# Optimization experiments

Hardware: AMD Instinct MI355X
Metric: run time of the kernel (lower is better)

The kernel has to match this reference:

```python
import jax, jax.numpy as jnp
import numpy as np

D_MODEL = 2048
D_FF = 8192
N_LOCAL = 8192


def _ffn(x, W1, b1, W2, b2):
    # ExpertFFN: Linear -> GELU(exact, torch default) -> Linear
    h = jax.nn.gelu(x @ W1 + b1, approximate=False)
    return h @ W2 + b2


def setup_inputs() -> dict:
    key = jax.random.key(0)
    ks = jax.random.split(key, 12)
    s1 = 1.0 / np.sqrt(D_MODEL)
    s2 = 1.0 / np.sqrt(D_FF)
    inp = {
        "x_local": jax.random.normal(ks[0], (N_LOCAL, D_MODEL), jnp.float32),
        "top2_exp_id": jax.random.randint(ks[1], (N_LOCAL, 2), 0, 2),
        "top2_weight": jax.random.uniform(ks[2], (N_LOCAL, 2), jnp.float32),
        # expert 0 params
        "W1_0": jax.random.uniform(ks[3], (D_MODEL, D_FF), jnp.float32, -s1, s1),
        "b1_0": jax.random.uniform(ks[4], (D_FF,), jnp.float32, -s1, s1),
        "W2_0": jax.random.uniform(ks[5], (D_FF, D_MODEL), jnp.float32, -s2, s2),
        "b2_0": jax.random.uniform(ks[6], (D_MODEL,), jnp.float32, -s2, s2),
        # expert 1 params
        "W1_1": jax.random.uniform(ks[7], (D_MODEL, D_FF), jnp.float32, -s1, s1),
        "b1_1": jax.random.uniform(ks[8], (D_FF,), jnp.float32, -s1, s1),
        "W2_1": jax.random.uniform(ks[9], (D_FF, D_MODEL), jnp.float32, -s2, s2),
        "b2_1": jax.random.uniform(ks[10], (D_MODEL,), jnp.float32, -s2, s2),
    }
    return inp


def reference(x_local, top2_exp_id, top2_weight,
              W1_0, b1_0, W2_0, b2_0, W1_1, b1_1, W2_1, b2_1):
    # Single-rank semantics of MoETop2TwoExpertsPerRank (world_size=1):
    # every token is dispatched to its two chosen local experts (ids in {0,1})
    # and results are combined weighted by the gate weights.
    y0 = _ffn(x_local, W1_0, b1_0, W2_0, b2_0)  # (N, d_model)
    y1 = _ffn(x_local, W1_1, b1_1, W2_1, b2_1)  # (N, d_model)
    # local expert id = global_eid % 2 (EPR=2); select per (token, slot)
    sel = (top2_exp_id % 2)[..., None].astype(x_local.dtype)  # (N, 2, 1)
    ys = jnp.stack([y0, y1], axis=1)  # not needed; use where instead
    per_slot = (1.0 - sel) * y0[:, None, :] + sel * y1[:, None, :]  # (N,2,d)
    y_out = jnp.sum(top2_weight[..., None] * per_slot, axis=1)
    return y_out
```

## Files before the change

kernel.cpp:

```cpp
#include <hip/hip_runtime.h>
#include <hip/hip_bf16.h>
#include <stdint.h>

#define DM 2048
#define DF 8192
#define NT 8192

typedef unsigned short u16;
typedef __attribute__((ext_vector_type(8))) __bf16 bf16x8;
typedef __attribute__((ext_vector_type(4))) float f32x4;

typedef __attribute__((address_space(1))) uint8_t ga_u8_t;
typedef __attribute__((address_space(3))) uint8_t lds_u8_t;

__device__ __forceinline__ void async_cp16(const void* g, void* l) {
  __builtin_amdgcn_global_load_lds((ga_u8_t*)g, (lds_u8_t*)l, 16, 0, 0);
}

__device__ __forceinline__ u16 f2b(float f) {
  unsigned int u = __builtin_bit_cast(unsigned int, f);
  u = (u + 0x7fffu + ((u >> 16) & 1u)) >> 16;
  return (u16)u;
}
__device__ __forceinline__ float gelu_f(float x) {
  return 0.5f * x * (1.0f + erff(x * 0.70710678118654752f));
}

__global__ void prep_wtok(const int* __restrict__ eid, const float* __restrict__ w,
                          float2* __restrict__ wtok, int n) {
  int i = blockIdx.x * blockDim.x + threadIdx.x;
  if (i >= n) return;
  float a = 0.f, b = 0.f;
  int e0 = eid[2 * i] & 1, e1 = eid[2 * i + 1] & 1;
  float w0 = w[2 * i], w1 = w[2 * i + 1];
  if (e0) b += w0; else a += w0;
  if (e1) b += w1; else a += w1;
  wtok[i] = make_float2(a, b);
}

__global__ void conv_f32_bf16(const float* __restrict__ in, u16* __restrict__ out,
                              int n4) {
  int i = blockIdx.x * blockDim.x + threadIdx.x;
  if (i >= n4) return;
  float4 v = reinterpret_cast<const float4*>(in)[i];
  ushort4 o;
  o.x = f2b(v.x); o.y = f2b(v.y); o.z = f2b(v.z); o.w = f2b(v.w);
  reinterpret_cast<ushort4*>(out)[i] = o;
}

__global__ void transpose_conv(const float* __restrict__ in, u16* __restrict__ out,
                               int R, int Cc) {
  __shared__ float tile[32][33];
  int tx = threadIdx.x & 31, ty = threadIdx.x >> 5;
  int r0 = blockIdx.y * 32, c0 = blockIdx.x * 32;
#pragma unroll
  for (int i = 0; i < 32; i += 8)
    tile[ty + i][tx] = in[(size_t)(r0 + ty + i) * Cc + c0 + tx];
  __syncthreads();
#pragma unroll
  for (int i = 0; i < 32; i += 8)
    out[(size_t)(c0 + ty + i) * R + r0 + tx] = f2b(tile[tx][ty + i]);
}

__global__ void fill_sentinel(float* p, int n) {
  int i = blockIdx.x * blockDim.x + threadIdx.x;
  if (i < n) p[i] = 0.125f;
}

template <int MODE>
__global__ void gemm_bt(const u16* __restrict__ A, const u16* __restrict__ Bt,
                        void* __restrict__ Cv, const float2* __restrict__ wtok,
                        const float* __restrict__ bias,
                        int M, int N, int K, int sel) {
  __shared__ __align__(16) u16 As[128 * 64];
  __shared__ __align__(16) u16 Bs[128 * 64];
  const int tid = threadIdx.x;
  const int wave = tid >> 6;
  const int lane = tid & 63;
  const int m0 = blockIdx.y * 128;
  const int n0 = blockIdx.x * 128;

  const int r8 = lane >> 3;
  const int p = lane & 7;
  const int q = p ^ r8;
  const u16* gA[4]; const u16* gB[4]; char* lA[4]; char* lB[4];
#pragma unroll
  for (int j = 0; j < 4; ++j) {
    int chunk = j * 4 + wave;
    int row = chunk * 8 + r8;
    gA[j] = A + (size_t)(m0 + row) * K + q * 8;
    gB[j] = Bt + (size_t)(n0 + row) * K + q * 8;
    lA[j] = (char*)As + chunk * 1024;
    lB[j] = (char*)Bs + chunk * 1024;
  }

  const int fr = lane & 15;
  const int qw = lane >> 4;
  const int wRow = (wave >> 1) * 64;
  const int wCol = (wave & 1) * 64;
  uint32_t aAddr[4], bAddr[4];
#pragma unroll
  for (int i = 0; i < 4; ++i) {
    int ra = wRow + i * 16 + fr;
    aAddr[i] = ra * 128 + ((qw ^ (ra & 7)) * 16);
    int rb = wCol + i * 16 + fr;
    bAddr[i] = rb * 128 + ((qw ^ (rb & 7)) * 16);
  }

  f32x4 acc[4][4] = {};

  for (int k0 = 0; k0 < K; k0 += 64) {
#pragma unroll
    for (int j = 0; j < 4; ++j) async_cp16(gA[j] + k0, lA[j]);
#pragma unroll
    for (int j = 0; j < 4; ++j) async_cp16(gB[j] + k0, lB[j]);
    __syncthreads();
#pragma unroll
    for (int kk = 0; kk < 2; ++kk) {
      const uint32_t kx = kk << 6;
      bf16x8 af[4], bfr[4];
#pragma unroll
      for (int i = 0; i < 4; ++i)
        af[i] = *reinterpret_cast<const bf16x8*>((const char*)As + (aAddr[i] ^ kx));
#pragma unroll
      for (int j = 0; j < 4; ++j)
        bfr[j] = *reinterpret_cast<const bf16x8*>((const char*)Bs + (bAddr[j] ^ kx));
#pragma unroll
      for (int i = 0; i < 4; ++i)
#pragma unroll
        for (int j = 0; j < 4; ++j)
          acc[i][j] = __builtin_amdgcn_mfma_f32_16x16x32_bf16(bfr[j], af[i],
                                                              acc[i][j], 0, 0, 0);
    }
    __syncthreads();
  }

#pragma unroll
  for (int i = 0; i < 4; ++i) {
    int t = m0 + wRow + i * 16 + fr;
    float2 wt = wtok[t];
    float ws = sel ? wt.y : wt.x;
#pragma unroll
    for (int j = 0; j < 4; ++j) {
      int col0 = n0 + wCol + j * 16 + qw * 4;
      float4 bb = *reinterpret_cast<const float4*>(bias + col0);
      f32x4 a = acc[i][j];
      if (MODE == 0) {
        u16* C = (u16*)Cv;
        ushort4 o;
        o.x = f2b(gelu_f(a.x + bb.x) * ws);
        o.y = f2b(gelu_f(a.y + bb.y) * ws);
        o.z = f2b(gelu_f(a.z + bb.z) * ws);
        o.w = f2b(gelu_f(a.w + bb.w) * ws);
        *reinterpret_cast<ushort4*>(C + (size_t)t * N + col0) = o;
      } else {
        float* C = (float*)Cv;
        float4 o;
        o.x = a.x + ws * bb.x;
        o.y = a.y + ws * bb.y;
        o.z = a.z + ws * bb.z;
        o.w = a.w + ws * bb.w;
        if (MODE == 2) {
          float4 pv = *reinterpret_cast<const float4*>(C + (size_t)t * N + col0);
          o.x += pv.x; o.y += pv.y; o.z += pv.z; o.w += pv.w;
        }
        *reinterpret_cast<float4*>(C + (size_t)t * N + col0) = o;
      }
    }
  }
}

extern "C" void kernel_launch(void* const* d_in, const int* in_sizes, int n_in,
                              void* d_out, int out_size, void* d_ws, size_t ws_size,
                              hipStream_t stream) {
  const float* x    = (const float*)d_in[0];
  const int*   eid  = (const int*)d_in[1];
  const float* topw = (const float*)d_in[2];
  const float* W1_0 = (const float*)d_in[3];
  const float* b1_0 = (const float*)d_in[4];
  const float* W2_0 = (const float*)d_in[5];
  const float* b2_0 = (const float*)d_in[6];
  const float* W1_1 = (const float*)d_in[7];
  const float* b1_1 = (const float*)d_in[8];
  const float* W2_1 = (const float*)d_in[9];
  const float* b2_1 = (const float*)d_in[10];
  float* out = (float*)d_out;

  char* ws = (char*)d_ws;
  const size_t SZ_WT = (size_t)DM * DF * sizeof(u16);
  size_t off = (size_t)NT * sizeof(float2);
  float2* wtok = (float2*)ws;
  u16* Xb  = (u16*)(ws + off); off += (size_t)NT * DM * sizeof(u16);
  u16* WTa = (u16*)(ws + off); off += SZ_WT;
  u16* WTb = (u16*)(ws + off); off += SZ_WT;
  u16* H   = (u16*)(ws + off); off += (size_t)NT * DF * sizeof(u16);

  if (ws_size < off) {
    fill_sentinel<<<(out_size + 255) / 256, 256, 0, stream>>>(out, out_size);
    return;
  }

  prep_wtok<<<(NT + 255) / 256, 256, 0, stream>>>(eid, topw, wtok, NT);
  conv_f32_bf16<<<(NT * DM / 4 + 255) / 256, 256, 0, stream>>>(x, Xb, NT * DM / 4);

  dim3 g1(DF / 128, NT / 128);
  dim3 g2(DM / 128, NT / 128);

  transpose_conv<<<dim3(DF / 32, DM / 32), 256, 0, stream>>>(W1_0, WTa, DM, DF);
  gemm_bt<0><<<g1, 256, 0, stream>>>(Xb, WTa, H, wtok, b1_0, NT, DF, DM, 0);
  transpose_conv<<<dim3(DM / 32, DF / 32), 256, 0, stream>>>(W2_0, WTb, DF, DM);
  gemm_bt<1><<<g2, 256, 0, stream>>>(H, WTb, out, wtok, b2_0, NT, DM, DF, 0);
  transpose_conv<<<dim3(DF / 32, DM / 32), 256, 0, stream>>>(W1_1, WTa, DM, DF);
  gemm_bt<0><<<g1, 256, 0, stream>>>(Xb, WTa, H, wtok, b1_1, NT, DF, DM, 1);
  transpose_conv<<<dim3(DM / 32, DF / 32), 256, 0, stream>>>(W2_1, WTb, DF, DM);
  gemm_bt<2><<<g2, 256, 0, stream>>>(H, WTb, out, wtok, b2_1, NT, DM, DF, 1);
}
```

Measured before the change: 1.429 ms.

## Rewrite GEMM as 256x256 tile, 8-wave, double-buffered pipelined kernel

Replaces the 128x128 single-buffered GEMM with a 256x256 tile run by 512 threads. Global-to-LDS loads are double-buffered and interleaved with four MFMA phases, using explicit waitcnt, sched_barrier and setprio. Workgroup IDs are swizzled to improve L2 reuse. The larger tile raises arithmetic intensity and hides load latency, but 128KB of LDS per block limits occupancy and adds register pressure.

Result: faster. 1.334 ms (-6.7%).

```diff
diff --git a/kernel.cpp b/kernel.cpp
--- a/kernel.cpp
+++ b/kernel.cpp
@@ -68,82 +68,179 @@
 }
 
 template <int MODE>
-__global__ void gemm_bt(const u16* __restrict__ A, const u16* __restrict__ Bt,
-                        void* __restrict__ Cv, const float2* __restrict__ wtok,
-                        const float* __restrict__ bias,
-                        int M, int N, int K, int sel) {
-  __shared__ __align__(16) u16 As[128 * 64];
-  __shared__ __align__(16) u16 Bs[128 * 64];
+__global__ __launch_bounds__(512, 2)
+void gemm_bt(const u16* __restrict__ A, const u16* __restrict__ Bt,
+             void* __restrict__ Cv, const float2* __restrict__ wtok,
+             const float* __restrict__ bias,
+             int M, int N, int K, int sel) {
+  __shared__ __align__(16) char smem[131072];
   const int tid = threadIdx.x;
-  const int wave = tid >> 6;
+  const int w = tid >> 6;
   const int lane = tid & 63;
-  const int m0 = blockIdx.y * 128;
-  const int n0 = blockIdx.x * 128;
-
-  const int r8 = lane >> 3;
-  const int p = lane & 7;
-  const int q = p ^ r8;
-  const u16* gA[4]; const u16* gB[4]; char* lA[4]; char* lB[4];
-#pragma unroll
-  for (int j = 0; j < 4; ++j) {
-    int chunk = j * 4 + wave;
-    int row = chunk * 8 + r8;
+
+  const int nwg = gridDim.x * gridDim.y;
+  const int wg = blockIdx.y * gridDim.x + blockIdx.x;
+  const int swz = (wg & 7) * (nwg >> 3) + (wg >> 3);
+  const int bx = swz % gridDim.x;
+  const int by = swz / gridDim.x;
+  const int m0 = by * 256;
+  const int n0 = bx * 256;
+  const int NKT = K >> 6;
+
+  const int r8 = lane >> 3, p8 = lane & 7, q = p8 ^ r8;
+  const u16* gA[2];
+  const u16* gB[2];
+  int ldsOff[2];
+#pragma unroll
+  for (int j = 0; j < 2; ++j) {
+    const int c = j * 8 + w;
+    const int row = c * 8 + r8;
     gA[j] = A + (size_t)(m0 + row) * K + q * 8;
     gB[j] = Bt + (size_t)(n0 + row) * K + q * 8;
-    lA[j] = (char*)As + chunk * 1024;
-    lB[j] = (char*)Bs + chunk * 1024;
+    ldsOff[j] = c * 1024;
   }
-
-  const int fr = lane & 15;
-  const int qw = lane >> 4;
-  const int wRow = (wave >> 1) * 64;
-  const int wCol = (wave & 1) * 64;
-  uint32_t aAddr[4], bAddr[4];
-#pragma unroll
-  for (int i = 0; i < 4; ++i) {
-    int ra = wRow + i * 16 + fr;
-    aAddr[i] = ra * 128 + ((qw ^ (ra & 7)) * 16);
-    int rb = wCol + i * 16 + fr;
-    bAddr[i] = rb * 128 + ((qw ^ (rb & 7)) * 16);
+  const size_t hstep = (size_t)128 * K;
+
+  auto stA = [&](int kt, int h, int bp) {
+    char* d = smem + bp * 65536 + h * 16384;
+    const size_t go = (size_t)h * hstep + (size_t)kt * 64;
+    async_cp16(gA[0] + go, d + ldsOff[0]);
+    async_cp16(gA[1] + go, d + ldsOff[1]);
+  };
+  auto stB = [&](int kt, int h, int bp) {
+    char* d = smem + 32768 + bp * 65536 + h * 16384;
+    const size_t go = (size_t)h * hstep + (size_t)kt * 64;
+    async_cp16(gB[0] + go, d + ldsOff[0]);
+    async_cp16(gB[1] + go, d + ldsOff[1]);
+  };
+
+  const int fr = lane & 15, qw = lane >> 4;
+  const int wr = w >> 2, wc = w & 3;
+  const int sw = (qw ^ (fr & 7)) << 4;
+  const uint32_t aBase = (uint32_t)((wr * 128 + fr) * 128 + sw);
+  const uint32_t bBase = (uint32_t)(32768 + (wc * 64 + fr) * 128 + sw);
+
+  auto ldf = [&](const char* base, uint32_t off) {
+    return *reinterpret_cast<const bf16x8*>(base + off);
+  };
+
+  f32x4 acc[8][4] = {};
+  bf16x8 af[4][2], bq[4][2];
+
+  stA(0, 0, 0); stA(0, 1, 0);
+  stB(0, 0, 0); stB(0, 1, 0);
+  stB(1, 0, 1); stB(1, 1, 1);
+  asm volatile("s_waitcnt vmcnt(4)" ::: "memory");
+  __builtin_amdgcn_s_barrier();
+
+  for (int t = 0; t < NKT; ++t) {
+    const int bp = t & 1;
+    const char* Ab = smem + bp * 65536;
+    const int kt1 = (t + 1 < NKT) ? t + 1 : NKT - 1;
+    const int kt2 = (t + 2 < NKT) ? t + 2 : NKT - 1;
+
+#pragma unroll
+    for (int i = 0; i < 4; ++i) {
+      af[i][0] = ldf(Ab, aBase + i * 2048);
+      af[i][1] = ldf(Ab, (aBase + i * 2048) ^ 64u);
+    }
+#pragma unroll
+    for (int j = 0; j < 2; ++j) {
+      bq[j][0] = ldf(Ab, bBase + j * 2048);
+      bq[j][1] = ldf(Ab, (bBase + j * 2048) ^ 64u);
+    }
+    stA(kt1, 0, bp ^ 1);
+    __builtin_amdgcn_sched_barrier(0);
+    __builtin_amdgcn_s_barrier();
+    asm volatile("s_waitcnt lgkmcnt(0)" ::: "memory");
+    __builtin_amdgcn_sched_barrier(0);
+    __builtin_amdgcn_s_setprio(1);
+#pragma unroll
+    for (int kk = 0; kk < 2; ++kk)
+#pragma unroll
+      for (int i = 0; i < 4; ++i)
+#pragma unroll
+        for (int j = 0; j < 2; ++j)
+          acc[i][j] = __builtin_amdgcn_mfma_f32_16x16x32_bf16(
+              bq[j][kk], af[i][kk], acc[i][j], 0, 0, 0);
+    __builtin_amdgcn_s_setprio(0);
+    __builtin_amdgcn_sched_barrier(0);
+    __builtin_amdgcn_s_barrier();
+
+#pragma unroll
+    for (int j = 2; j < 4; ++j) {
+      bq[j][0] = ldf(Ab, bBase + j * 2048);
+      bq[j][1] = ldf(Ab, (bBase + j * 2048) ^ 64u);
+    }
+    stA(kt1, 1, bp ^ 1);
+    __builtin_amdgcn_sched_barrier(0);
+    __builtin_amdgcn_s_barrier();
+    asm volatile("s_waitcnt lgkmcnt(0)" ::: "memory");
+    __builtin_amdgcn_sched_barrier(0);
+    __builtin_amdgcn_s_setprio(1);
+#pragma unroll
+    for (int kk = 0; kk < 2; ++kk)
+#pragma unroll
+      for (int i = 0; i < 4; ++i)
+#pragma unroll
+        for (int j = 2; j < 4; ++j)
+          acc[i][j] = __builtin_amdgcn_mfma_f32_16x16x32_bf16(
+              bq[j][kk], af[i][kk], acc[i][j], 0, 0, 0);
+    __builtin_amdgcn_s_setprio(0);
+    __builtin_amdgcn_sched_barrier(0);
+    __builtin_amdgcn_s_barrier();
+
+#pragma unroll
+    for (int i = 0; i < 4; ++i) {
+      af[i][0] = ldf(Ab, aBase + (i + 4) * 2048);
+      af[i][1] = ldf(Ab, (aBase + (i + 4) * 2048) ^ 64u);
+    }
+    stB(kt2, 0, bp);
+    __builtin_amdgcn_sched_barrier(0);
+    __builtin_amdgcn_s_barrier();
+    asm volatile("s_waitcnt lgkmcnt(0)" ::: "memory");
+    __builtin_amdgcn_sched_barrier(0);
+    __builtin_amdgcn_s_setprio(1);
+#pragma unroll
+    for (int kk = 0; kk < 2; ++kk)
+#pragma unroll
+      for (int i = 0; i < 4; ++i)
+#pragma unroll
+        for (int j = 2; j < 4; ++j)
+          acc[i + 4][j] = __builtin_amdgcn_mfma_f32_16x16x32_bf16(
+              bq[j][kk], af[i][kk], acc[i + 4][j], 0, 0, 0);
+    __builtin_amdgcn_s_setprio(0);
+    __builtin_amdgcn_sched_barrier(0);
+    __builtin_amdgcn_s_barrier();
+
+    stB(kt2, 1, bp);
+    __builtin_amdgcn_sched_barrier(0);
+    __builtin_amdgcn_s_setprio(1);
+#pragma unroll
+    for (int kk = 0; kk < 2; ++kk)
+#pragma unroll
+      for (int i = 0; i < 4; ++i)
+#pragma unroll
+        for (int j = 0; j < 2; ++j)
+          acc[i + 4][j] = __builtin_amdgcn_mfma_f32_16x16x32_bf16(
+              bq[j][kk], af[i][kk], acc[i + 4][j], 0, 0, 0);
+    __builtin_amdgcn_s_setprio(0);
+    __builtin_amdgcn_sched_barrier(0);
+    asm volatile("s_waitcnt vmcnt(4)" ::: "memory");
+    __builtin_amdgcn_sched_barrier(0);
+    __builtin_amdgcn_s_barrier();
   }
-
-  f32x4 acc[4][4] = {};
-
-  for (int k0 = 0; k0 < K; k0 += 64) {
-#pragma unroll
-    for (int j = 0; j < 4; ++j) async_cp16(gA[j] + k0, lA[j]);
-#pragma unroll
-    for (int j = 0; j < 4; ++j) async_cp16(gB[j] + k0, lB[j]);
-    __syncthreads();
-#pragma unroll
-    for (int kk = 0; kk < 2; ++kk) {
-      const uint32_t kx = kk << 6;
-      bf16x8 af[4], bfr[4];
-#pragma unroll
-      for (int i = 0; i < 4; ++i)
-        af[i] = *reinterpret_cast<const bf16x8*>((const char*)As + (aAddr[i] ^ kx));
-#pragma unroll
-      for (int j = 0; j < 4; ++j)
-        bfr[j] = *reinterpret_cast<const bf16x8*>((const char*)Bs + (bAddr[j] ^ kx));
-#pragma unroll
-      for (int i = 0; i < 4; ++i)
-#pragma unroll
-        for (int j = 0; j < 4; ++j)
-          acc[i][j] = __builtin_amdgcn_mfma_f32_16x16x32_bf16(bfr[j], af[i],
-                                                              acc[i][j], 0, 0, 0);
-    }
-    __syncthreads();
-  }
-
-#pragma unroll
-  for (int i = 0; i < 4; ++i) {
-    int t = m0 + wRow + i * 16 + fr;
-    float2 wt = wtok[t];
-    float ws = sel ? wt.y : wt.x;
+  asm volatile("s_waitcnt vmcnt(0)" ::: "memory");
+
+#pragma unroll
+  for (int i = 0; i < 8; ++i) {
+    const int trow = m0 + wr * 128 + i * 16 + fr;
+    const float2 wt = wtok[trow];
+    const float ws = sel ? wt.y : wt.x;
 #pragma unroll
     for (int j = 0; j < 4; ++j) {
-      int col0 = n0 + wCol + j * 16 + qw * 4;
-      float4 bb = *reinterpret_cast<const float4*>(bias + col0);
+      const int col0 = n0 + wc * 64 + j * 16 + qw * 4;
+      const float4 bb = *reinterpret_cast<const float4*>(bias + col0);
       f32x4 a = acc[i][j];
       if (MODE == 0) {
         u16* C = (u16*)Cv;
@@ -152,7 +249,7 @@
         o.y = f2b(gelu_f(a.y + bb.y) * ws);
         o.z = f2b(gelu_f(a.z + bb.z) * ws);
         o.w = f2b(gelu_f(a.w + bb.w) * ws);
-        *reinterpret_cast<ushort4*>(C + (size_t)t * N + col0) = o;
+        *reinterpret_cast<ushort4*>(C + (size_t)trow * N + col0) = o;
       } else {
         float* C = (float*)Cv;
         float4 o;
@@ -161,10 +258,10 @@
         o.z = a.z + ws * bb.z;
         o.w = a.w + ws * bb.w;
         if (MODE == 2) {
-          float4 pv = *reinterpret_cast<const float4*>(C + (size_t)t * N + col0);
+          float4 pv = *reinterpret_cast<const float4*>(C + (size_t)trow * N + col0);
           o.x += pv.x; o.y += pv.y; o.z += pv.z; o.w += pv.w;
         }
-        *reinterpret_cast<float4*>(C + (size_t)t * N + col0) = o;
+        *reinterpret_cast<float4*>(C + (size_t)trow * N + col0) = o;
       }
     }
   }
@@ -203,15 +300,15 @@
   prep_wtok<<<(NT + 255) / 256, 256, 0, stream>>>(eid, topw, wtok, NT);
   conv_f32_bf16<<<(NT * DM / 4 + 255) / 256, 256, 0, stream>>>(x, Xb, NT * DM / 4);
 
-  dim3 g1(DF / 128, NT / 128);
-  dim3 g2(DM / 128, NT / 128);
+  dim3 g1(DF / 256, NT / 256);
+  dim3 g2(DM / 256, NT / 256);
 
   transpose_conv<<<dim3(DF / 32, DM / 32), 256, 0, stream>>>(W1_0, WTa, DM, DF);
-  gemm_bt<0><<<g1, 256, 0, stream>>>(Xb, WTa, H, wtok, b1_0, NT, DF, DM, 0);
+  gemm_bt<0><<<g1, 512, 0, stream>>>(Xb, WTa, H, wtok, b1_0, NT, DF, DM, 0);
   transpose_conv<<<dim3(DM / 32, DF / 32), 256, 0, stream>>>(W2_0, WTb, DF, DM);
-  gemm_bt<1><<<g2, 256, 0, stream>>>(H, WTb, out, wtok, b2_0, NT, DM, DF, 0);
+  gemm_bt<1><<<g2, 512, 0, stream>>>(H, WTb, out, wtok, b2_0, NT, DM, DF, 0);
   transpose_conv<<<dim3(DF / 32, DM / 32), 256, 0, stream>>>(W1_1, WTa, DM, DF);
-  gemm_bt<0><<<g1, 256, 0, stream>>>(Xb, WTa, H, wtok, b1_1, NT, DF, DM, 1);
+  gemm_bt<0><<<g1, 512, 0, stream>>>(Xb, WTa, H, wtok, b1_1, NT, DF, DM, 1);
   transpose_conv<<<dim3(DM / 32, DF / 32), 256, 0, stream>>>(W2_1, WTb, DF, DM);
-  gemm_bt<2><<<g2, 256, 0, stream>>>(H, WTb, out, wtok, b2_1, NT, DM, DF, 1);
-}
+  gemm_bt<2><<<g2, 512, 0, stream>>>(H, WTb, out, wtok, b2_1, NT, DM, DF, 1);
+}
```
